# Kernel optimization log

Measured on AMD Instinct MI355X. Metric: run time of the kernel, lower is better.

## Reference

```python
import jax, jax.numpy as jnp
import numpy as np

CONF_THRES = 0.8
NMS_THRES = 0.4
MAX_DET = 300          # fixed capacity for jit-compatible NMS output
N_BOXES = 262144
N_CLASSES = 80


def xywh2xyxy(x):
    xy, wh = x[..., :2], x[..., 2:4]
    return jnp.concatenate([xy - wh * 0.5, xy + wh * 0.5], axis=-1)


def bbox_iou(box, boxes):
    # one box [4] vs many [N,4]; original uses the +1 pixel-area convention
    x1 = jnp.maximum(box[0], boxes[:, 0])
    y1 = jnp.maximum(box[1], boxes[:, 1])
    x2 = jnp.minimum(box[2], boxes[:, 2])
    y2 = jnp.minimum(box[3], boxes[:, 3])
    inter = jnp.clip(x2 - x1 + 1, 0) * jnp.clip(y2 - y1 + 1, 0)
    a1 = (box[2] - box[0] + 1) * (box[3] - box[1] + 1)
    a2 = (boxes[:, 2] - boxes[:, 0] + 1) * (boxes[:, 3] - boxes[:, 1] + 1)
    return inter / (a1 + a2 - inter + 1e-16)


def nms_single(pred):
    # pred: [N, 85] raw YOLO output for one image
    boxes = xywh2xyxy(pred[:, :4])
    obj = pred[:, 4]
    cls_scores = pred[:, 5:]
    class_conf = cls_scores.max(axis=-1)
    class_pred = jnp.argmax(cls_scores, axis=-1).astype(pred.dtype)
    valid = obj >= CONF_THRES
    score = obj * class_conf
    # sort valid boxes by descending score; invalid pushed to the end
    order = jnp.argsort(jnp.where(valid, -score, jnp.inf))
    det = jnp.concatenate(
        [boxes, obj[:, None], class_conf[:, None], class_pred[:, None]], axis=1
    )[order]  # [N, 7] = x1,y1,x2,y2,obj,class_conf,class_pred
    valid = valid[order]

    def step(valid, _):
        idx = jnp.argmax(valid)            # first still-valid (= highest score)
        any_valid = jnp.any(valid)
        cur = det[idx]
        iou = bbox_iou(cur[:4], det[:, :4])
        invalid = (iou > NMS_THRES) & (det[:, 6] == cur[6]) & valid
        # weighted box merge over the suppressed group (as in original NMS)
        w = jnp.where(invalid, det[:, 4], 0.0)
        merged = (w[:, None] * det[:, :4]).sum(0) / (w.sum() + 1e-16)
        out = jnp.where(any_valid,
                        jnp.concatenate([merged, cur[4:]]),
                        jnp.zeros(7, pred.dtype))
        return valid & ~invalid, (out, any_valid)

    _, (kept, kept_valid) = jax.lax.scan(step, valid, None, length=MAX_DET)
    return kept, kept_valid  # [MAX_DET,7], [MAX_DET]


def setup_inputs() -> dict:
    key = jax.random.key(0)
    detections = jax.random.uniform(key, (1, N_BOXES, 5 + N_CLASSES), dtype=jnp.float32)
    return {"detections": detections}


def reference(detections):
    kept, kv = nms_single(detections[0])
    d = kept[:, 5:]                        # [MAX_DET, 2] = (class_conf, class_pred)
    conf_key = jnp.where(kv, d[:, 0], -jnp.inf)  # padded rows sort to the end
    order = jnp.argsort(conf_key)          # ascending (torch argsort)
    d = d[order][::-1]                     # torch.flip -> descending class_conf
    kv = kv[order][::-1]
    probs = jnp.where(kv, d[:, 0], 0.0)    # self.probs
    ids = d[:, 1][None, :]                 # self.ids, shape [1, MAX_DET]
    return ids, probs
```

## Files before the change

### kernel.cpp

```cpp
#include <hip/hip_runtime.h>

#pragma clang fp contract(off)

#define NBOX 262144
#define NCLS 80
#define ROWS 85
#define CAP 1024
#define POOL 8192
#define VMAX 65536
#define G 256

typedef unsigned long long ull;

__global__ __launch_bounds__(64) void k_init(int* __restrict__ vcount,
                                             int* __restrict__ pool_count) {
    if (threadIdx.x == 0) { *vcount = 0; *pool_count = 0; }
}

__global__ __launch_bounds__(256) void k_stage1(const float* __restrict__ det,
                                                int* __restrict__ vcount,
                                                int* __restrict__ cls_v,
                                                ull* __restrict__ key_v,
                                                float* __restrict__ conf_v,
                                                float4* __restrict__ box_v) {
    __shared__ int s_wl[256];
    __shared__ float s_obj[256];
    __shared__ int wsum[4];
    __shared__ int s_base, s_nv;
    const int t = threadIdx.x, lane = t & 63, wave = t >> 6;
    const int bi = blockIdx.x * 256 + t;

    float obj = det[(size_t)bi * ROWS + 4];
    bool valid = (obj >= 0.8f);
    ull m = __ballot(valid);
    if (lane == 0) wsum[wave] = (int)__popcll(m);
    __syncthreads();
    if (t == 0) {
        int s = 0;
        #pragma unroll
        for (int w = 0; w < 4; w++) { int cc = wsum[w]; wsum[w] = s; s += cc; }
        s_nv = s;
        s_base = s ? atomicAdd(vcount, s) : 0;
    }
    __syncthreads();
    if (valid) {
        int r = wsum[wave] + (int)__popcll(m & ((1ull << lane) - 1ull));
        s_wl[r] = t;
        s_obj[r] = obj;
    }
    __syncthreads();
    const int nv = s_nv, base = s_base;

    const int grp = t >> 4, c = t & 15;
    for (int r0 = 0; r0 < nv; r0 += 16) {
        int widx = r0 + grp;
        if (widx < nv) {
            int b = s_wl[widx];
            const float* p = det + (size_t)(blockIdx.x * 256 + b) * ROWS;
            float aux = (c < 5) ? p[c] : 0.0f;
            float v0 = p[5 + c];
            float v1 = p[21 + c];
            float v2 = p[37 + c];
            float v3 = p[53 + c];
            float v4 = p[69 + c];
            float mv = v0; int mj = c;
            if (v1 > mv) { mv = v1; mj = 16 + c; }
            if (v2 > mv) { mv = v2; mj = 32 + c; }
            if (v3 > mv) { mv = v3; mj = 48 + c; }
            if (v4 > mv) { mv = v4; mj = 64 + c; }
            #pragma unroll
            for (int off = 8; off; off >>= 1) {
                float ov = __shfl_xor(mv, off);
                int oj = __shfl_xor(mj, off);
                if (ov > mv || (ov == mv && oj < mj)) { mv = ov; mj = oj; }
            }
            int gb = lane & 48;
            float x = __shfl(aux, gb + 0);
            float y = __shfl(aux, gb + 1);
            float w = __shfl(aux, gb + 2);
            float h = __shfl(aux, gb + 3);
            if (c == 0) {
                float ob = s_obj[widx];
                float score = ob * mv;
                float hw = w * 0.5f, hh = h * 0.5f;
                int gi = blockIdx.x * 256 + b;
                int pos = base + widx;
                if (pos < VMAX) {
                    cls_v[pos] = mj;
                    key_v[pos] = ((ull)(~__float_as_uint(score)) << 32) | (unsigned)gi;
                    conf_v[pos] = mv;
                    box_v[pos] = make_float4(x - hw, y - hh, x + hw, y + hh);
                }
            }
        }
    }
}

__global__ __launch_bounds__(256) void k_hist(const int* __restrict__ vcount,
                                              const int* __restrict__ cls_v,
                                              int* __restrict__ ghist) {
    __shared__ int h[NCLS];
    const int t = threadIdx.x, g = blockIdx.x;
    if (t < NCLS) h[t] = 0;
    __syncthreads();
    const int total = min(*vcount, VMAX);
    const int seg = (total + G - 1) / G;
    int idx = g * seg + t;
    if (t < seg && idx < total) atomicAdd(&h[cls_v[idx]], 1);
    __syncthreads();
    if (t < NCLS) ghist[t * G + g] = h[t];
}

__global__ __launch_bounds__(1024) void k_offsets(int* __restrict__ ghist,
                                                  int* __restrict__ cstart,
                                                  int* __restrict__ ccount) {
    __shared__ int ctot[NCLS];
    __shared__ int cst[NCLS];
    const int t = threadIdx.x, wave = t >> 6, lane = t & 63;
    for (int cb = wave; cb < NCLS; cb += 16) {
        int bse = cb * G + lane * 4;
        int v0 = ghist[bse], v1 = ghist[bse + 1], v2 = ghist[bse + 2], v3 = ghist[bse + 3];
        int s = v0 + v1 + v2 + v3;
        int inc = s;
        #pragma unroll
        for (int off = 1; off < 64; off <<= 1) {
            int o = __shfl_up(inc, off);
            if (lane >= off) inc += o;
        }
        int ex = inc - s;
        ghist[bse] = ex;
        ghist[bse + 1] = ex + v0;
        ghist[bse + 2] = ex + v0 + v1;
        ghist[bse + 3] = ex + v0 + v1 + v2;
        if (lane == 63) ctot[cb] = inc;
    }
    __syncthreads();
    if (t == 0) {
        int s = 0;
        for (int cc = 0; cc < NCLS; cc++) { cst[cc] = s; s += ctot[cc]; }
    }
    __syncthreads();
    for (int i = t; i < NCLS * G; i += 1024) ghist[i] += cst[i >> 8];
    if (t < NCLS) { cstart[t] = cst[t]; ccount[t] = ctot[t]; }
}

__global__ __launch_bounds__(256) void k_scatter(const int* __restrict__ vcount,
                                                 const int* __restrict__ cls_v,
                                                 const ull* __restrict__ key_v,
                                                 const float* __restrict__ conf_v,
                                                 const float4* __restrict__ box_v,
                                                 const int* __restrict__ ghist,
                                                 ull* __restrict__ key2,
                                                 float* __restrict__ conf2,
                                                 float4* __restrict__ box2) {
    __shared__ int cnt[NCLS];
    const int t = threadIdx.x, g = blockIdx.x;
    if (t < NCLS) cnt[t] = 0;
    __syncthreads();
    const int total = min(*vcount, VMAX);
    const int seg = (total + G - 1) / G;
    int idx = g * seg + t;
    if (t < seg && idx < total) {
        int cc = cls_v[idx];
        int r = atomicAdd(&cnt[cc], 1);
        int dest = ghist[cc * G + g] + r;
        key2[dest] = key_v[idx];
        conf2[dest] = conf_v[idx];
        box2[dest] = box_v[idx];
    }
}

template <int L>
__device__ __forceinline__ int exact_alive(ull (&k)[L]) {
    int a = 0;
    #pragma unroll
    for (int j = 0; j < L; j++) a += (int)__popcll(__ballot(k[j] != ~0ULL));
    return a;
}

template <int L>
__device__ __forceinline__ void pick_loop(ull (&k)[L], float4 (&bx)[L], float (&cf)[L],
                                          int lane, int& alive, int& np,
                                          ull* pkey, float* pconf, int stopAt) {
    while (alive > stopAt) {
        ull lm = k[0]; int lj = 0;
        #pragma unroll
        for (int j = 1; j < L; j++) if (k[j] < lm) { lm = k[j]; lj = j; }
        ull gm = lm;
        #pragma unroll
        for (int off = 32; off; off >>= 1) { ull o = __shfl_xor(gm, off); if (o < gm) gm = o; }
        if (gm == ~0ULL) { alive = 0; break; }
        float4 cb = bx[0]; float cc = cf[0];
        #pragma unroll
        for (int j = 1; j < L; j++) if (j == lj) { cb = bx[j]; cc = cf[j]; }
        ull wb = __ballot(lm == gm);
        int wl2 = (int)__ffsll((long long)wb) - 1;
        cb.x = __shfl(cb.x, wl2); cb.y = __shfl(cb.y, wl2);
        cb.z = __shfl(cb.z, wl2); cb.w = __shfl(cb.w, wl2);
        cc = __shfl(cc, wl2);
        if (lane == 0) { pkey[np] = gm; pconf[np] = cc; }
        np++;
        float a1 = (cb.z - cb.x + 1.0f) * (cb.w - cb.y + 1.0f);
        #pragma unroll
        for (int j = 0; j < L; j++) {
            if (k[j] != ~0ULL) {
                float4 b = bx[j];
                float xx1 = fmaxf(cb.x, b.x), yy1 = fmaxf(cb.y, b.y);
                float xx2 = fminf(cb.z, b.z), yy2 = fminf(cb.w, b.w);
                float iw = xx2 - xx1 + 1.0f, ih = yy2 - yy1 + 1.0f;
                float inter = fmaxf(iw, 0.0f) * fmaxf(ih, 0.0f);
                float a2 = (b.z - b.x + 1.0f) * (b.w - b.y + 1.0f);
                float iou = inter / (a1 + a2 - inter + 1e-16f);
                if (iou > 0.4f) k[j] = ~0ULL;
            }
        }
        if ((np & 7) == 0) alive = exact_alive(k);
    }
}

template <int LF, int LT>
__device__ __forceinline__ void compact_regs(ull (&k)[LF], float4 (&bx)[LF], float (&cf)[LF],
                                             ull (&k2)[LT], float4 (&b2)[LT], float (&c2)[LT],
                                             int lane, int alive,
                                             ull* dk, float4* db, float* dc) {
    int ci = 0;
    #pragma unroll
    for (int j = 0; j < LF; j++) if (k[j] != ~0ULL) ci++;
    int inc = ci;
    for (int off = 1; off < 64; off <<= 1) {
        int o = __shfl_up(inc, off);
        if (lane >= off) inc += o;
    }
    int wp = inc - ci;
    #pragma unroll
    for (int j = 0; j < LF; j++)
        if (k[j] != ~0ULL) { dk[wp] = k[j]; db[wp] = bx[j]; dc[wp] = cf[j]; wp++; }
    #pragma unroll
    for (int j = 0; j < LT; j++) {
        int pos = lane + (j << 6);
        bool ok = pos < alive;
        k2[j] = ok ? dk[pos] : ~0ULL;
        b2[j] = ok ? db[pos] : make_float4(0.f, 0.f, 0.f, 0.f);
        c2[j] = ok ? dc[pos] : 0.0f;
    }
}

__global__ __launch_bounds__(64) void k_nms(const int* __restrict__ cstart,
                                            const int* __restrict__ ccount,
                                            const ull* __restrict__ key2,
                                            const float* __restrict__ conf2,
                                            const float4* __restrict__ box2,
                                            ull* __restrict__ pool_key,
                                            float* __restrict__ pool_conf,
                                            int* __restrict__ pool_cls,
                                            int* __restrict__ pool_count) {
    __shared__ ull sk[CAP];
    __shared__ float4 sb[CAP];
    __shared__ float sc[CAP];
    __shared__ ull pkey[CAP];
    __shared__ float pconf[CAP];
    const int c = blockIdx.x, lane = threadIdx.x;
    const int n = min(ccount[c], CAP);
    const int s0 = cstart[c];

    ull k16[16]; float4 b16[16]; float c16[16];
    #pragma unroll
    for (int j = 0; j < 16; j++) {
        int pos = lane + (j << 6);
        bool ok = pos < n;
        k16[j] = ok ? key2[s0 + pos] : ~0ULL;
        b16[j] = ok ? box2[s0 + pos] : make_float4(0.f, 0.f, 0.f, 0.f);
        c16[j] = ok ? conf2[s0 + pos] : 0.0f;
    }
    int alive = n, np = 0;
    pick_loop<16>(k16, b16, c16, lane, alive, np, pkey, pconf, 256);
    alive = exact_alive(k16);
    ull k4[4]; float4 b4[4]; float c4[4];
    compact_regs<16, 4>(k16, b16, c16, k4, b4, c4, lane, alive, sk, sb, sc);
    pick_loop<4>(k4, b4, c4, lane, alive, np, pkey, pconf, 64);
    alive = exact_alive(k4);
    ull k1[1]; float4 b1[1]; float c1[1];
    compact_regs<4, 1>(k4, b4, c4, k1, b1, c1, lane, alive, sk, sb, sc);
    pick_loop<1>(k1, b1, c1, lane, alive, np, pkey, pconf, 0);

    int npw = min(np, 300);
    int base = 0;
    if (lane == 0 && npw) base = atomicAdd(pool_count, npw);
    base = __shfl(base, 0);
    for (int j = lane; j < npw; j += 64) {
        int pp = base + j;
        if (pp < POOL) {
            ull gm = pkey[j];
            pool_key[pp] = ((ull)((unsigned)(gm >> 32) & 0x7FFFFFFFu) << 32)
                         | ((gm & 0xFFFFFFFFull) << 14) | (ull)pp;
            pool_conf[pp] = pconf[j];
            pool_cls[pp] = c;
        }
    }
}

__device__ __forceinline__ void bsort512(ull (&x)[8], int lane) {
    #pragma unroll
    for (int k = 2; k <= 512; k <<= 1) {
        #pragma unroll
        for (int j = k >> 1; j >= 64; j >>= 1) {
            const int jr = j >> 6;
            #pragma unroll
            for (int r2 = 0; r2 < 8; r2++) {
                if ((r2 & jr) == 0) {
                    const bool asc = (((r2 << 6) & k) == 0);
                    ull a = x[r2], b = x[r2 | jr];
                    if ((a > b) == asc) { x[r2] = b; x[r2 | jr] = a; }
                }
            }
        }
        #pragma unroll
        for (int j = ((k >> 1) > 32 ? 32 : (k >> 1)); j >= 1; j >>= 1) {
            #pragma unroll
            for (int r2 = 0; r2 < 8; r2++) {
                int i = (r2 << 6) + lane;
                bool asc = ((i & k) == 0);
                ull o = __shfl_xor(x[r2], j);
                bool lower = ((lane & j) == 0);
                ull mn = x[r2] < o ? x[r2] : o;
                ull mx2 = x[r2] < o ? o : x[r2];
                x[r2] = (asc == lower) ? mn : mx2;
            }
        }
    }
}

__global__ __launch_bounds__(256) void k_final(const ull* __restrict__ pool_key,
                                               const float* __restrict__ pool_conf,
                                               const int* __restrict__ pool_cls,
                                               const int* __restrict__ pool_count,
                                               float* __restrict__ out) {
    __shared__ int s_red[4];
    __shared__ int s_stat[2];
    __shared__ ull s_mm[8];
    __shared__ ull s_buf[512];
    __shared__ unsigned s_cb[512];
    __shared__ unsigned s_cl[512];
    const int t = threadIdx.x, wave = t >> 6, lane = t & 63;
    const int K = min(*pool_count, POOL);
    ull key[32];
    #pragma unroll
    for (int j = 0; j < 32; j++) {
        int pos = t + (j << 8);
        key[j] = (pos < K) ? pool_key[pos] : ~0ULL;
    }

    const bool selAll = (K <= 511);
    int bsh = 63; ull p = 0;
    if (!selAll) {
        ull mn = ~0ULL, mx = 0;
        #pragma unroll
        for (int j = 0; j < 32; j++) {
            ull kk = key[j];
            if (kk != ~0ULL) { if (kk < mn) mn = kk; if (kk > mx) mx = kk; }
        }
        #pragma unroll
        for (int off = 32; off; off >>= 1) {
            ull on = __shfl_xor(mn, off), ox = __shfl_xor(mx, off);
            if (on < mn) mn = on;
            if (ox > mx) mx = ox;
        }
        if (lane == 0) { s_mm[wave * 2] = mn; s_mm[wave * 2 + 1] = mx; }
        __syncthreads();
        mn = min(min(s_mm[0], s_mm[2]), min(s_mm[4], s_mm[6]));
        mx = max(max(s_mm[1], s_mm[3]), max(s_mm[5], s_mm[7]));
        ull diff = mn ^ mx;
        int hb = 63 - __builtin_clzll(diff);
        int r = 300, cand = K, b = hb;
        p = mn >> (hb + 1);
        while (b >= 13 && cand > 212) {
            int c0 = 0;
            #pragma unroll
            for (int j = 0; j < 32; j++) {
                ull kk = key[j];
                if ((kk >> (b + 1)) == p && (((kk >> b) & 1ull) == 0)) c0++;
            }
            #pragma unroll
            for (int off = 32; off; off >>= 1) c0 += __shfl_xor(c0, off);
            if (lane == 0) s_red[wave] = c0;
            __syncthreads();
            if (t == 0) s_stat[0] = s_red[0] + s_red[1] + s_red[2] + s_red[3];
            __syncthreads();
            int cnt0 = s_stat[0];
            if (r <= cnt0) { cand = cnt0; p = p << 1; }
            else { r -= cnt0; cand -= cnt0; p = (p << 1) | 1ull; }
            b--;
        }
        bsh = b + 1;
    }

    if (t == 0) s_stat[1] = 0;
    __syncthreads();
    int ci = 0;
    #pragma unroll
    for (int j = 0; j < 32; j++) {
        ull kk = key[j];
        bool sel = selAll ? ((kk >> 63) == 0) : ((kk >> bsh) <= p);
        if (sel) ci++;
    }
    int inc = ci;
    for (int off = 1; off < 64; off <<= 1) {
        int o = __shfl_up(inc, off);
        if (lane >= off) inc += o;
    }
    int wtot = __shfl(inc, 63);
    int wbase2 = 0;
    if (lane == 0 && wtot) wbase2 = atomicAdd(&s_stat[1], wtot);
    wbase2 = __shfl(wbase2, 0);
    int wp = wbase2 + inc - ci;
    #pragma unroll
    for (int j = 0; j < 32; j++) {
        ull kk = key[j];
        bool sel = selAll ? ((kk >> 63) == 0) : ((kk >> bsh) <= p);
        if (sel) s_buf[wp++] = kk;
    }
    __syncthreads();
    const int S = s_stat[1];
    for (int i = t; i < 512; i += 256) if (i >= S) s_buf[i] = ~0ULL;
    __syncthreads();
    if (wave != 0) return;

    #pragma clang loop unroll(disable)
    for (int pass = 0; pass < 2; pass++) {
        ull x[8];
        #pragma unroll
        for (int r2 = 0; r2 < 8; r2++) x[r2] = s_buf[(r2 << 6) + lane];
        bsort512(x, lane);
        if (pass == 0) {
            #pragma unroll
            for (int r2 = 0; r2 < 8; r2++) {
                int i = (r2 << 6) + lane;
                ull kk = x[r2];
                ull k2 = ~0ULL;
                if (i < 300 && kk != ~0ULL) {
                    int pidx = (int)(kk & 0x3FFFull);
                    unsigned cb = __float_as_uint(pool_conf[pidx]);
                    unsigned cl = (unsigned)pool_cls[pidx];
                    s_cb[i] = cb; s_cl[i] = cl;
                    k2 = ((ull)(~cb) << 32) | (unsigned)(~i);
                }
                s_buf[i] = k2;
            }
        } else {
            #pragma unroll
            for (int r2 = 0; r2 < 8; r2++) {
                int i = (r2 << 6) + lane;
                if (i < 300) {
                    ull kk = x[r2];
                    float idv = 0.0f, pv = 0.0f;
                    if (kk != ~0ULL) {
                        int slot = (int)(~(unsigned)(kk & 0xFFFFFFFFull));
                        pv = __uint_as_float(s_cb[slot]);
                        idv = (float)(int)s_cl[slot];
                    }
                    out[i] = idv;
                    out[300 + i] = pv;
                }
            }
        }
    }
}

extern "C" void kernel_launch(void* const* d_in, const int* in_sizes, int n_in,
                              void* d_out, int out_size, void* d_ws, size_t ws_size,
                              hipStream_t stream) {
    const float* det = (const float*)d_in[0];
    float* out = (float*)d_out;
    char* ws = (char*)d_ws;

    int* vcount = (int*)(ws + 0);
    int* pool_count = (int*)(ws + 4);
    int* cls_v = (int*)(ws + 64);
    ull* key_v = (ull*)(ws + 262208);
    float* conf_v = (float*)(ws + 786496);
    float4* box_v = (float4*)(ws + 1048640);
    ull* pool_key = (ull*)(ws + 2097216);
    float* pool_conf = (float*)(ws + 2162752);
    int* pool_cls = (int*)(ws + 2195520);
    int* ghist = (int*)(ws + 2228288);
    int* cstart = (int*)(ws + 2310208);
    int* ccount = (int*)(ws + 2310528);
    ull* key2 = (ull*)(ws + 2310912);
    float* conf2 = (float*)(ws + 2835200);
    float4* box2 = (float4*)(ws + 3097344);

    k_init<<<1, 64, 0, stream>>>(vcount, pool_count);
    k_stage1<<<NBOX / 256, 256, 0, stream>>>(det, vcount, cls_v, key_v, conf_v, box_v);
    k_hist<<<G, 256, 0, stream>>>(vcount, cls_v, ghist);
    k_offsets<<<1, 1024, 0, stream>>>(ghist, cstart, ccount);
    k_scatter<<<G, 256, 0, stream>>>(vcount, cls_v, key_v, conf_v, box_v, ghist,
                                     key2, conf2, box2);
    k_nms<<<NCLS, 64, 0, stream>>>(cstart, ccount, key2, conf2, box2,
                                   pool_key, pool_conf, pool_cls, pool_count);
    k_final<<<1, 256, 0, stream>>>(pool_key, pool_conf, pool_cls, pool_count, out);
}
```

Measured before the change: 194.6 us.

## Scatter valid boxes directly into per-class buckets via global atomics

Stage 1 now increments a per-class counter with a global atomic and writes each valid detection straight into a fixed 1024-slot bucket for its class. This removes the histogram, prefix-offset and scatter kernels along with their intermediate buffers and launches. The NMS pick loop also stops once 300 boxes are kept in a class. The trade-offs are contention on 80 global atomics, a nondeterministic order within each bucket (the sort keys still order picks), and silent truncation of any class with more than 1024 candidates.

```diff
diff --git a/kernel.cpp b/kernel.cpp
--- a/kernel.cpp
+++ b/kernel.cpp
@@ -7,26 +7,25 @@
 #define ROWS 85
 #define CAP 1024
 #define POOL 8192
-#define VMAX 65536
-#define G 256
 
 typedef unsigned long long ull;
 
-__global__ __launch_bounds__(64) void k_init(int* __restrict__ vcount,
-                                             int* __restrict__ pool_count) {
-    if (threadIdx.x == 0) { *vcount = 0; *pool_count = 0; }
+__global__ __launch_bounds__(128) void k_init(int* __restrict__ ccount,
+                                              int* __restrict__ pool_count) {
+    const int t = threadIdx.x;
+    if (t < NCLS) ccount[t] = 0;
+    if (t == NCLS) *pool_count = 0;
 }
 
 __global__ __launch_bounds__(256) void k_stage1(const float* __restrict__ det,
-                                                int* __restrict__ vcount,
-                                                int* __restrict__ cls_v,
-                                                ull* __restrict__ key_v,
-                                                float* __restrict__ conf_v,
-                                                float4* __restrict__ box_v) {
+                                                int* __restrict__ ccount,
+                                                ull* __restrict__ key2,
+                                                float* __restrict__ conf2,
+                                                float4* __restrict__ box2) {
     __shared__ int s_wl[256];
     __shared__ float s_obj[256];
     __shared__ int wsum[4];
-    __shared__ int s_base, s_nv;
+    __shared__ int s_nv;
     const int t = threadIdx.x, lane = t & 63, wave = t >> 6;
     const int bi = blockIdx.x * 256 + t;
 
@@ -40,7 +39,6 @@
         #pragma unroll
         for (int w = 0; w < 4; w++) { int cc = wsum[w]; wsum[w] = s; s += cc; }
         s_nv = s;
-        s_base = s ? atomicAdd(vcount, s) : 0;
     }
     __syncthreads();
     if (valid) {
@@ -49,7 +47,7 @@
         s_obj[r] = obj;
     }
     __syncthreads();
-    const int nv = s_nv, base = s_base;
+    const int nv = s_nv;
 
     const int grp = t >> 4, c = t & 15;
     for (int r0 = 0; r0 < nv; r0 += 16) {
@@ -84,89 +82,15 @@
                 float score = ob * mv;
                 float hw = w * 0.5f, hh = h * 0.5f;
                 int gi = blockIdx.x * 256 + b;
-                int pos = base + widx;
-                if (pos < VMAX) {
-                    cls_v[pos] = mj;
-                    key_v[pos] = ((ull)(~__float_as_uint(score)) << 32) | (unsigned)gi;
-                    conf_v[pos] = mv;
-                    box_v[pos] = make_float4(x - hw, y - hh, x + hw, y + hh);
+                int r = atomicAdd(&ccount[mj], 1);
+                if (r < CAP) {
+                    int pos = (mj << 10) + r;
+                    key2[pos] = ((ull)(~__float_as_uint(score)) << 32) | (unsigned)gi;
+                    conf2[pos] = mv;
+                    box2[pos] = make_float4(x - hw, y - hh, x + hw, y + hh);
                 }
             }
         }
-    }
-}
-
-__global__ __launch_bounds__(256) void k_hist(const int* __restrict__ vcount,
-                                              const int* __restrict__ cls_v,
-                                              int* __restrict__ ghist) {
-    __shared__ int h[NCLS];
-    const int t = threadIdx.x, g = blockIdx.x;
-    if (t < NCLS) h[t] = 0;
-    __syncthreads();
-    const int total = min(*vcount, VMAX);
-    const int seg = (total + G - 1) / G;
-    int idx = g * seg + t;
-    if (t < seg && idx < total) atomicAdd(&h[cls_v[idx]], 1);
-    __syncthreads();
-    if (t < NCLS) ghist[t * G + g] = h[t];
-}
-
-__global__ __launch_bounds__(1024) void k_offsets(int* __restrict__ ghist,
-                                                  int* __restrict__ cstart,
-                                                  int* __restrict__ ccount) {
-    __shared__ int ctot[NCLS];
-    __shared__ int cst[NCLS];
-    const int t = threadIdx.x, wave = t >> 6, lane = t & 63;
-    for (int cb = wave; cb < NCLS; cb += 16) {
-        int bse = cb * G + lane * 4;
-        int v0 = ghist[bse], v1 = ghist[bse + 1], v2 = ghist[bse + 2], v3 = ghist[bse + 3];
-        int s = v0 + v1 + v2 + v3;
-        int inc = s;
-        #pragma unroll
-        for (int off = 1; off < 64; off <<= 1) {
-            int o = __shfl_up(inc, off);
-            if (lane >= off) inc += o;
-        }
-        int ex = inc - s;
-        ghist[bse] = ex;
-        ghist[bse + 1] = ex + v0;
-        ghist[bse + 2] = ex + v0 + v1;
-        ghist[bse + 3] = ex + v0 + v1 + v2;
-        if (lane == 63) ctot[cb] = inc;
-    }
-    __syncthreads();
-    if (t == 0) {
-        int s = 0;
-        for (int cc = 0; cc < NCLS; cc++) { cst[cc] = s; s += ctot[cc]; }
-    }
-    __syncthreads();
-    for (int i = t; i < NCLS * G; i += 1024) ghist[i] += cst[i >> 8];
-    if (t < NCLS) { cstart[t] = cst[t]; ccount[t] = ctot[t]; }
-}
-
-__global__ __launch_bounds__(256) void k_scatter(const int* __restrict__ vcount,
-                                                 const int* __restrict__ cls_v,
-                                                 const ull* __restrict__ key_v,
-                                                 const float* __restrict__ conf_v,
-                                                 const float4* __restrict__ box_v,
-                                                 const int* __restrict__ ghist,
-                                                 ull* __restrict__ key2,
-                                                 float* __restrict__ conf2,
-                                                 float4* __restrict__ box2) {
-    __shared__ int cnt[NCLS];
-    const int t = threadIdx.x, g = blockIdx.x;
-    if (t < NCLS) cnt[t] = 0;
-    __syncthreads();
-    const int total = min(*vcount, VMAX);
-    const int seg = (total + G - 1) / G;
-    int idx = g * seg + t;
-    if (t < seg && idx < total) {
-        int cc = cls_v[idx];
-        int r = atomicAdd(&cnt[cc], 1);
-        int dest = ghist[cc * G + g] + r;
-        key2[dest] = key_v[idx];
-        conf2[dest] = conf_v[idx];
-        box2[dest] = box_v[idx];
     }
 }
 
@@ -182,7 +106,7 @@
 __device__ __forceinline__ void pick_loop(ull (&k)[L], float4 (&bx)[L], float (&cf)[L],
                                           int lane, int& alive, int& np,
                                           ull* pkey, float* pconf, int stopAt) {
-    while (alive > stopAt) {
+    while (alive > stopAt && np < 300) {
         ull lm = k[0]; int lj = 0;
         #pragma unroll
         for (int j = 1; j < L; j++) if (k[j] < lm) { lm = k[j]; lj = j; }
@@ -245,8 +169,7 @@
     }
 }
 
-__global__ __launch_bounds__(64) void k_nms(const int* __restrict__ cstart,
-                                            const int* __restrict__ ccount,
+__global__ __launch_bounds__(64) void k_nms(const int* __restrict__ ccount,
                                             const ull* __restrict__ key2,
                                             const float* __restrict__ conf2,
                                             const float4* __restrict__ box2,
@@ -261,7 +184,7 @@
     __shared__ float pconf[CAP];
     const int c = blockIdx.x, lane = threadIdx.x;
     const int n = min(ccount[c], CAP);
-    const int s0 = cstart[c];
+    const int s0 = c << 10;
 
     ull k16[16]; float4 b16[16]; float c16[16];
     #pragma unroll
@@ -473,29 +396,18 @@
     float* out = (float*)d_out;
     char* ws = (char*)d_ws;
 
-    int* vcount = (int*)(ws + 0);
-    int* pool_count = (int*)(ws + 4);
-    int* cls_v = (int*)(ws + 64);
-    ull* key_v = (ull*)(ws + 262208);
-    float* conf_v = (float*)(ws + 786496);
-    float4* box_v = (float4*)(ws + 1048640);
-    ull* pool_key = (ull*)(ws + 2097216);
-    float* pool_conf = (float*)(ws + 2162752);
-    int* pool_cls = (int*)(ws + 2195520);
-    int* ghist = (int*)(ws + 2228288);
-    int* cstart = (int*)(ws + 2310208);
-    int* ccount = (int*)(ws + 2310528);
-    ull* key2 = (ull*)(ws + 2310912);
-    float* conf2 = (float*)(ws + 2835200);
-    float4* box2 = (float4*)(ws + 3097344);
-
-    k_init<<<1, 64, 0, stream>>>(vcount, pool_count);
-    k_stage1<<<NBOX / 256, 256, 0, stream>>>(det, vcount, cls_v, key_v, conf_v, box_v);
-    k_hist<<<G, 256, 0, stream>>>(vcount, cls_v, ghist);
-    k_offsets<<<1, 1024, 0, stream>>>(ghist, cstart, ccount);
-    k_scatter<<<G, 256, 0, stream>>>(vcount, cls_v, key_v, conf_v, box_v, ghist,
-                                     key2, conf2, box2);
-    k_nms<<<NCLS, 64, 0, stream>>>(cstart, ccount, key2, conf2, box2,
+    int* ccount = (int*)(ws + 0);
+    int* pool_count = (int*)(ws + 320);
+    ull* key2 = (ull*)(ws + 384);
+    float* conf2 = (float*)(ws + 655744);
+    float4* box2 = (float4*)(ws + 983424);
+    ull* pool_key = (ull*)(ws + 2294144);
+    float* pool_conf = (float*)(ws + 2359680);
+    int* pool_cls = (int*)(ws + 2392448);
+
+    k_init<<<1, 128, 0, stream>>>(ccount, pool_count);
+    k_stage1<<<NBOX / 256, 256, 0, stream>>>(det, ccount, key2, conf2, box2);
+    k_nms<<<NCLS, 64, 0, stream>>>(ccount, key2, conf2, box2,
                                    pool_key, pool_conf, pool_cls, pool_count);
     k_final<<<1, 256, 0, stream>>>(pool_key, pool_conf, pool_cls, pool_count, out);
 }
```

After: 316.8 us. +62.8%, slower.
